# Kernel optimization log

Hardware: AMD Instinct MI355X
Metric: run time of the kernel (lower is better)

## Reference

```python
import jax, jax.numpy as jnp
import numpy as np

N_NODES = 100000
N_EDGES = 1600000
IN_CH = 128


def _sage_conv(x, src, dst, Wl, b, Wr, n_nodes):
    # PyG SAGEConv (aggr='mean', root_weight=True):
    #   out_i = lin_l(mean_{j->i} x_j) + lin_r(x_i)
    msg = x[src]                                             # [E, F]
    agg = jax.ops.segment_sum(msg, dst, num_segments=n_nodes)  # [N, F]
    deg = jax.ops.segment_sum(jnp.ones((src.shape[0],), x.dtype), dst,
                              num_segments=n_nodes)          # [N]
    mean = agg / jnp.maximum(deg, 1.0)[:, None]
    return mean @ Wl + b + x @ Wr


def setup_inputs() -> dict:
    key = jax.random.key(0)
    ks = jax.random.split(key, 10)
    x = jax.random.normal(ks[0], (N_NODES, IN_CH), dtype=jnp.float32)
    edge_index = jax.random.randint(ks[1], (2, N_EDGES), 0, N_NODES, dtype=jnp.int64)
    s = 0.05
    return {
        "x": x,
        "edge_index": edge_index,
        "W1l": jax.random.normal(ks[2], (IN_CH, 32), dtype=jnp.float32) * s,
        "b1": jax.random.normal(ks[3], (32,), dtype=jnp.float32) * s,
        "W1r": jax.random.normal(ks[4], (IN_CH, 32), dtype=jnp.float32) * s,
        "W2l": jax.random.normal(ks[5], (32, 16), dtype=jnp.float32) * s,
        "b2": jax.random.normal(ks[6], (16,), dtype=jnp.float32) * s,
        "W2r": jax.random.normal(ks[7], (32, 16), dtype=jnp.float32) * s,
        "Wfc": jax.random.normal(ks[8], (16, 2), dtype=jnp.float32) * s,
        "bfc": jax.random.normal(ks[9], (2,), dtype=jnp.float32) * s,
    }


def reference(x, edge_index, W1l, b1, W1r, W2l, b2, W2r, Wfc, bfc):
    src, dst = edge_index[0], edge_index[1]
    n = x.shape[0]
    h = jax.nn.relu(_sage_conv(x, src, dst, W1l, b1, W1r, n))   # [N, 32]
    h = jax.nn.relu(_sage_conv(h, src, dst, W2l, b2, W2r, n))   # [N, 16]
    return h @ Wfc + bfc                                        # [N, 2]
```

## Files before the change

### kernel.cpp

```cpp
#include <hip/hip_runtime.h>

#define TPB 256
#define BK_SHIFT 7
#define BK_SIZE 128
#define NBK_MAX 800
#define EPT 32
#define CAP 3072

typedef __attribute__((ext_vector_type(8))) short bf16x8;
typedef __attribute__((ext_vector_type(4))) float f32x4;

__device__ __forceinline__ unsigned short f2bf(float f) {
    unsigned u = __float_as_uint(f);
    unsigned r = (u + 0x7FFFu + ((u >> 16) & 1u)) >> 16;
    return (unsigned short)r;
}
__device__ __forceinline__ float bf2f(unsigned short b) {
    return __uint_as_float((unsigned)b << 16);
}
__device__ __forceinline__ void acc4(float4& a, ushort4 v) {
    a.x += bf2f(v.x); a.y += bf2f(v.y); a.z += bf2f(v.z); a.w += bf2f(v.w);
}

__global__ __launch_bounds__(256) void hist_buckets(
    const int* __restrict__ dst, int* __restrict__ bcnt, int E, int NBK)
{
    __shared__ int h[NBK_MAX];
    const int t = threadIdx.x;
    for (int i = t; i < NBK; i += 256) h[i] = 0;
    __syncthreads();
    const int E4 = E >> 2;
    for (int e4 = blockIdx.x * blockDim.x + t; e4 < E4; e4 += gridDim.x * blockDim.x) {
        int4 d = ((const int4*)dst)[e4];
        atomicAdd(&h[d.x >> BK_SHIFT], 1);
        atomicAdd(&h[d.y >> BK_SHIFT], 1);
        atomicAdd(&h[d.z >> BK_SHIFT], 1);
        atomicAdd(&h[d.w >> BK_SHIFT], 1);
    }
    if (blockIdx.x == 0) {
        for (int e = E4 * 4 + t; e < E; e += 256)
            atomicAdd(&h[dst[e] >> BK_SHIFT], 1);
    }
    __syncthreads();
    for (int i = t; i < NBK; i += 256)
        if (h[i]) atomicAdd(&bcnt[i], h[i]);
}

__global__ __launch_bounds__(1024) void scan_buckets(
    const int* __restrict__ bcnt, int* __restrict__ bbase,
    int* __restrict__ gcursor, int NBK)
{
    __shared__ int s[1024];
    const int t = threadIdx.x;
    int v = (t < NBK) ? bcnt[t] : 0;
    s[t] = v;
    __syncthreads();
    for (int off = 1; off < 1024; off <<= 1) {
        int u = (t >= off) ? s[t - off] : 0;
        __syncthreads();
        s[t] += u;
        __syncthreads();
    }
    if (t < NBK) {
        int excl = s[t] - v;
        bbase[t]   = excl;
        gcursor[t] = excl;
    }
}

__global__ __launch_bounds__(256) void bin_scatter(
    const int* __restrict__ src, const int* __restrict__ dst,
    int* __restrict__ gcursor, int* __restrict__ pk, int E, int NBK)
{
    __shared__ int lcnt[NBK_MAX];
    __shared__ int lbase[NBK_MAX];
    __shared__ int lrank[NBK_MAX];
    const int t = threadIdx.x;
    const int e0 = blockIdx.x * (256 * EPT);

    for (int i = t; i < NBK; i += 256) { lcnt[i] = 0; lrank[i] = 0; }
    __syncthreads();

    #pragma unroll 4
    for (int k = 0; k < EPT; ++k) {
        int e = e0 + k * 256 + t;
        if (e < E) atomicAdd(&lcnt[dst[e] >> BK_SHIFT], 1);
    }
    __syncthreads();

    for (int i = t; i < NBK; i += 256) {
        int c = lcnt[i];
        if (c) lbase[i] = atomicAdd(&gcursor[i], c);
    }
    __syncthreads();

    #pragma unroll 4
    for (int k = 0; k < EPT; ++k) {
        int e = e0 + k * 256 + t;
        if (e < E) {
            int d = dst[e], s = src[e];
            int b = d >> BK_SHIFT;
            int r = atomicAdd(&lrank[b], 1);
            pk[lbase[b] + r] = (s << BK_SHIFT) | (d & (BK_SIZE - 1));
        }
    }
}

__global__ __launch_bounds__(256) void gemm1_mfma(
    const float* __restrict__ A,
    const float* __restrict__ Wl,
    const float* __restrict__ Wr,
    const float* __restrict__ b,
    unsigned short* __restrict__ Yb,
    float* __restrict__ C,
    int N)
{
    const int lane = threadIdx.x & 63;
    const int m    = lane & 15;
    const int quad = lane >> 4;
    const int wave   = blockIdx.x * (blockDim.x >> 6) + (threadIdx.x >> 6);
    const int nwaves = gridDim.x * (blockDim.x >> 6);
    const int ntiles = (N + 15) >> 4;

    bf16x8 Bf[4][4];
    #pragma unroll
    for (int kc = 0; kc < 4; ++kc) {
        #pragma unroll
        for (int jt = 0; jt < 4; ++jt) {
            const float* W = (jt < 2) ? Wl : Wr;
            const int col = (jt & 1) * 16 + m;
            #pragma unroll
            for (int j = 0; j < 8; ++j) {
                int k = kc * 32 + quad * 8 + j;
                Bf[kc][jt][j] = (short)f2bf(W[k * 32 + col]);
            }
        }
    }

    const float bias0 = b[m];
    const float bias1 = b[16 + m];

    for (int tile = wave; tile < ntiles; tile += nwaves) {
        const int node0 = tile * 16;
        const int gn = node0 + m;
        const bool okA = gn < N;
        const float* rowp = A + (size_t)gn * 128;

        bf16x8 Af[4];
        #pragma unroll
        for (int kc = 0; kc < 4; ++kc) {
            float4 v0 = make_float4(0.f, 0.f, 0.f, 0.f);
            float4 v1 = make_float4(0.f, 0.f, 0.f, 0.f);
            if (okA) {
                v0 = *(const float4*)&rowp[kc * 32 + quad * 8];
                v1 = *(const float4*)&rowp[kc * 32 + quad * 8 + 4];
            }
            Af[kc][0] = (short)f2bf(v0.x); Af[kc][1] = (short)f2bf(v0.y);
            Af[kc][2] = (short)f2bf(v0.z); Af[kc][3] = (short)f2bf(v0.w);
            Af[kc][4] = (short)f2bf(v1.x); Af[kc][5] = (short)f2bf(v1.y);
            Af[kc][6] = (short)f2bf(v1.z); Af[kc][7] = (short)f2bf(v1.w);
        }

        f32x4 acc[4] = {{0.f,0.f,0.f,0.f},{0.f,0.f,0.f,0.f},
                        {0.f,0.f,0.f,0.f},{0.f,0.f,0.f,0.f}};
        #pragma unroll
        for (int kc = 0; kc < 4; ++kc) {
            #pragma unroll
            for (int jt = 0; jt < 4; ++jt)
                acc[jt] = __builtin_amdgcn_mfma_f32_16x16x32_bf16(
                    Af[kc], Bf[kc][jt], acc[jt], 0, 0, 0);
        }

        const int nodeBase = node0 + quad * 4;
        #pragma unroll
        for (int reg = 0; reg < 4; ++reg) {
            const int node = nodeBase + reg;
            if (node < N) {
                Yb[(size_t)node * 32 + m]      = f2bf(acc[0][reg]);
                Yb[(size_t)node * 32 + 16 + m] = f2bf(acc[1][reg]);
                C [(size_t)node * 32 + m]      = acc[2][reg] + bias0;
                C [(size_t)node * 32 + 16 + m] = acc[3][reg] + bias1;
            }
        }
    }
}

__global__ __launch_bounds__(256) void gather_gemm2(
    const int* __restrict__ bbase, const int* __restrict__ bcnt,
    const int* __restrict__ pk,
    const unsigned short* __restrict__ Yb,
    const float* __restrict__ c1,
    const float* __restrict__ W2l, const float* __restrict__ W2r,
    const float* __restrict__ b2,
    float* __restrict__ invdeg,
    unsigned short* __restrict__ y2b, float* __restrict__ c2, int N)
{
    __shared__ int lcnt[BK_SIZE];
    __shared__ int soff[BK_SIZE];
    __shared__ int wcur[BK_SIZE];
    __shared__ int sidx[CAP];

    const int t = threadIdx.x;
    const int b = blockIdx.x;
    const int base = bbase[b];
    const int cnt  = min(bcnt[b], CAP);
    const int node0 = b * BK_SIZE;

    if (t < BK_SIZE) lcnt[t] = 0;
    __syncthreads();

    for (int j = t; j < cnt; j += 256)
        atomicAdd(&lcnt[pk[base + j] & (BK_SIZE - 1)], 1);
    __syncthreads();

    int v = (t < BK_SIZE) ? lcnt[t] : 0;
    if (t < BK_SIZE) soff[t] = v;
    __syncthreads();
    for (int off = 1; off < BK_SIZE; off <<= 1) {
        int u = (t < BK_SIZE && t >= off) ? soff[t - off] : 0;
        __syncthreads();
        if (t < BK_SIZE) soff[t] += u;
        __syncthreads();
    }
    if (t < BK_SIZE) wcur[t] = soff[t] - v;
    __syncthreads();

    for (int j = t; j < cnt; j += 256) {
        int pv = pk[base + j];
        int d  = pv & (BK_SIZE - 1);
        int pos = atomicAdd(&wcur[d], 1);
        sidx[pos] = pv >> BK_SHIFT;
    }
    __syncthreads();

    const int q = t & 7;
    #pragma unroll
    for (int pass = 0; pass < 4; ++pass) {
        const int nl = pass * 32 + (t >> 3);
        const int node = node0 + nl;
        const bool active = node < N;
        float h[4] = {0.f, 0.f, 0.f, 0.f};
        if (active) {
            const int deg = lcnt[nl];
            const int en  = soff[nl];
            const int st  = en - deg;
            const float w = 1.0f / fmaxf((float)deg, 1.0f);
            if (q == 0) invdeg[node] = w;

            float4 a0 = make_float4(0.f,0.f,0.f,0.f);
            float4 a1 = make_float4(0.f,0.f,0.f,0.f);
            float4 a2 = make_float4(0.f,0.f,0.f,0.f);
            float4 a3 = make_float4(0.f,0.f,0.f,0.f);
            int j = st;
            for (; j + 3 < en; j += 4) {
                int s0 = sidx[j], s1 = sidx[j+1], s2 = sidx[j+2], s3 = sidx[j+3];
                ushort4 v0 = *(const ushort4*)&Yb[(size_t)s0 * 32 + q * 4];
                ushort4 v1 = *(const ushort4*)&Yb[(size_t)s1 * 32 + q * 4];
                ushort4 v2 = *(const ushort4*)&Yb[(size_t)s2 * 32 + q * 4];
                ushort4 v3 = *(const ushort4*)&Yb[(size_t)s3 * 32 + q * 4];
                acc4(a0, v0); acc4(a1, v1); acc4(a2, v2); acc4(a3, v3);
            }
            for (; j < en; ++j) {
                ushort4 vv = *(const ushort4*)&Yb[(size_t)sidx[j] * 32 + q * 4];
                acc4(a0, vv);
            }
            float4 acc;
            acc.x = (a0.x + a1.x) + (a2.x + a3.x);
            acc.y = (a0.y + a1.y) + (a2.y + a3.y);
            acc.z = (a0.z + a1.z) + (a2.z + a3.z);
            acc.w = (a0.w + a1.w) + (a2.w + a3.w);

            float4 c = *(const float4*)&c1[(size_t)node * 32 + q * 4];
            h[0] = fmaxf(c.x + acc.x * w, 0.f);
            h[1] = fmaxf(c.y + acc.y * w, 0.f);
            h[2] = fmaxf(c.z + acc.z * w, 0.f);
            h[3] = fmaxf(c.w + acc.w * w, 0.f);
        }

        const int  j0  = q * 4;
        const bool isY = (j0 < 16);
        const int  jj  = isY ? j0 : (j0 - 16);
        const float* Wb = isY ? W2l : W2r;

        float o0 = 0.f, o1 = 0.f, o2 = 0.f, o3 = 0.f;
        #pragma unroll
        for (int k = 0; k < 32; ++k) {
            float hk = __shfl(h[k & 3], k >> 2, 8);
            float4 wv = *(const float4*)&Wb[k * 16 + jj];
            o0 += hk * wv.x; o1 += hk * wv.y; o2 += hk * wv.z; o3 += hk * wv.w;
        }

        if (active) {
            if (isY) {
                ushort4 r;
                r.x = f2bf(o0); r.y = f2bf(o1); r.z = f2bf(o2); r.w = f2bf(o3);
                *(ushort4*)&y2b[(size_t)node * 16 + jj] = r;
            } else {
                float4 bb = *(const float4*)&b2[jj];
                *(float4*)&c2[(size_t)node * 16 + jj] =
                    make_float4(o0 + bb.x, o1 + bb.y, o2 + bb.z, o3 + bb.w);
            }
        }
    }
}

__global__ __launch_bounds__(256) void gather_final(
    const int* __restrict__ bbase, const int* __restrict__ bcnt,
    const int* __restrict__ pk,
    const unsigned short* __restrict__ Yb,
    const float* __restrict__ c2,
    const float* __restrict__ invdeg,
    const float* __restrict__ Wfc,
    const float* __restrict__ bfc,
    float* __restrict__ out, int N)
{
    __shared__ int lcnt[BK_SIZE];
    __shared__ int soff[BK_SIZE];
    __shared__ int wcur[BK_SIZE];
    __shared__ int sidx[CAP];

    const int t = threadIdx.x;
    const int b = blockIdx.x;
    const int base = bbase[b];
    const int cnt  = min(bcnt[b], CAP);
    const int node0 = b * BK_SIZE;

    if (t < BK_SIZE) lcnt[t] = 0;
    __syncthreads();

    for (int j = t; j < cnt; j += 256)
        atomicAdd(&lcnt[pk[base + j] & (BK_SIZE - 1)], 1);
    __syncthreads();

    int v = (t < BK_SIZE) ? lcnt[t] : 0;
    if (t < BK_SIZE) soff[t] = v;
    __syncthreads();
    for (int off = 1; off < BK_SIZE; off <<= 1) {
        int u = (t < BK_SIZE && t >= off) ? soff[t - off] : 0;
        __syncthreads();
        if (t < BK_SIZE) soff[t] += u;
        __syncthreads();
    }
    if (t < BK_SIZE) wcur[t] = soff[t] - v;
    __syncthreads();

    for (int j = t; j < cnt; j += 256) {
        int pv = pk[base + j];
        int d  = pv & (BK_SIZE - 1);
        int pos = atomicAdd(&wcur[d], 1);
        sidx[pos] = pv >> BK_SHIFT;
    }
    __syncthreads();

    const int q = t & 3;
    #pragma unroll
    for (int pass = 0; pass < 2; ++pass) {
        const int nl = pass * 64 + (t >> 2);
        const int node = node0 + nl;
        if (node < N) {
            const int deg = lcnt[nl];
            const int en  = soff[nl];
            const int st  = en - deg;
            const float w = invdeg[node];

            float4 a0 = make_float4(0.f,0.f,0.f,0.f);
            float4 a1 = make_float4(0.f,0.f,0.f,0.f);
            float4 a2 = make_float4(0.f,0.f,0.f,0.f);
            float4 a3 = make_float4(0.f,0.f,0.f,0.f);
            int j = st;
            for (; j + 3 < en; j += 4) {
                int s0 = sidx[j], s1 = sidx[j+1], s2 = sidx[j+2], s3 = sidx[j+3];
                ushort4 v0 = *(const ushort4*)&Yb[(size_t)s0 * 16 + q * 4];
                ushort4 v1 = *(const ushort4*)&Yb[(size_t)s1 * 16 + q * 4];
                ushort4 v2 = *(const ushort4*)&Yb[(size_t)s2 * 16 + q * 4];
                ushort4 v3 = *(const ushort4*)&Yb[(size_t)s3 * 16 + q * 4];
                acc4(a0, v0); acc4(a1, v1); acc4(a2, v2); acc4(a3, v3);
            }
            for (; j < en; ++j) {
                ushort4 vv = *(const ushort4*)&Yb[(size_t)sidx[j] * 16 + q * 4];
                acc4(a0, vv);
            }
            float4 acc;
            acc.x = (a0.x + a1.x) + (a2.x + a3.x);
            acc.y = (a0.y + a1.y) + (a2.y + a3.y);
            acc.z = (a0.z + a1.z) + (a2.z + a3.z);
            acc.w = (a0.w + a1.w) + (a2.w + a3.w);

            float4 c = *(const float4*)&c2[(size_t)node * 16 + q * 4];
            float h0 = fmaxf(c.x + acc.x * w, 0.f);
            float h1 = fmaxf(c.y + acc.y * w, 0.f);
            float h2 = fmaxf(c.z + acc.z * w, 0.f);
            float h3 = fmaxf(c.w + acc.w * w, 0.f);

            const float* Wq = &Wfc[q * 8];
            float o0 = h0 * Wq[0] + h1 * Wq[2] + h2 * Wq[4] + h3 * Wq[6];
            float o1 = h0 * Wq[1] + h1 * Wq[3] + h2 * Wq[5] + h3 * Wq[7];

            o0 += __shfl_xor(o0, 1); o0 += __shfl_xor(o0, 2);
            o1 += __shfl_xor(o1, 1); o1 += __shfl_xor(o1, 2);

            if (q == 0) ((float2*)out)[node] = make_float2(o0 + bfc[0], o1 + bfc[1]);
        } else {
            float z = 0.f;
            z += __shfl_xor(z, 1); z += __shfl_xor(z, 2);
        }
    }
}

extern "C" void kernel_launch(void* const* d_in, const int* in_sizes, int n_in,
                              void* d_out, int out_size, void* d_ws, size_t ws_size,
                              hipStream_t stream)
{
    const float* x   = (const float*)d_in[0];
    const int*   ei  = (const int*)d_in[1];
    const float* W1l = (const float*)d_in[2];
    const float* b1  = (const float*)d_in[3];
    const float* W1r = (const float*)d_in[4];
    const float* W2l = (const float*)d_in[5];
    const float* b2  = (const float*)d_in[6];
    const float* W2r = (const float*)d_in[7];
    const float* Wfc = (const float*)d_in[8];
    const float* bfc = (const float*)d_in[9];
    float* out = (float*)d_out;

    const int N = in_sizes[0] / 128;
    const int E = in_sizes[1] / 2;
    const int* src = ei;
    const int* dst = ei + E;

    const int NBK = (N + BK_SIZE - 1) / BK_SIZE;

    int*   bucket_cnt  = (int*)d_ws;
    int*   bucket_base = bucket_cnt + NBK_MAX;
    int*   gcursor     = bucket_base + NBK_MAX;
    float* invdeg      = (float*)(gcursor + NBK_MAX);
    int*   pk          = (int*)(invdeg + N);
    unsigned short* y1b = (unsigned short*)(pk + E);
    float* c1          = (float*)(y1b + (size_t)N * 32);
    unsigned short* y2b = (unsigned short*)(c1 + (size_t)N * 32);
    float* c2          = (float*)(y2b + (size_t)N * 16);

    hipMemsetAsync(bucket_cnt, 0, (size_t)NBK * sizeof(int), stream);
    hist_buckets<<<196, 256, 0, stream>>>(dst, bucket_cnt, E, NBK);
    scan_buckets<<<1, 1024, 0, stream>>>(bucket_cnt, bucket_base, gcursor, NBK);
    {
        int nb = (E + 256 * EPT - 1) / (256 * EPT);
        bin_scatter<<<nb, 256, 0, stream>>>(src, dst, gcursor, pk, E, NBK);
    }

    gemm1_mfma<<<256, TPB, 0, stream>>>(x, W1l, W1r, b1, y1b, c1, N);

    gather_gemm2<<<NBK, TPB, 0, stream>>>(
        bucket_base, bucket_cnt, pk, y1b, c1, W2l, W2r, b2,
        invdeg, y2b, c2, N);

    gather_final<<<NBK, TPB, 0, stream>>>(
        bucket_base, bucket_cnt, pk, y2b, c2, invdeg, Wfc, bfc, out, N);
}
```

Measured before the change: 214.1 us.

## Replace bucketed edge binning with per-node global CSR built via atomics

Swaps the 128-node bucket binning, which both gather kernels re-sorted in shared memory, for a full per-node CSR. A global per-node histogram, a block-level scan with an atomic global base, and an atomic scatter produce it once. The gather kernels then read row_start/degree directly, drop their per-block shared-memory sort and the invdeg buffer, and launch many more small blocks. The cost is about 3.2M global atomics on 100K counters, with contention and scattered writes, and node rows are no longer placed in ascending node order.

```diff
diff --git a/kernel.cpp b/kernel.cpp
--- a/kernel.cpp
+++ b/kernel.cpp
@@ -1,11 +1,6 @@
 #include <hip/hip_runtime.h>
 
 #define TPB 256
-#define BK_SHIFT 7
-#define BK_SIZE 128
-#define NBK_MAX 800
-#define EPT 32
-#define CAP 3072
 
 typedef __attribute__((ext_vector_type(8))) short bf16x8;
 typedef __attribute__((ext_vector_type(4))) float f32x4;
@@ -22,86 +17,69 @@
     a.x += bf2f(v.x); a.y += bf2f(v.y); a.z += bf2f(v.z); a.w += bf2f(v.w);
 }
 
-__global__ __launch_bounds__(256) void hist_buckets(
-    const int* __restrict__ dst, int* __restrict__ bcnt, int E, int NBK)
-{
-    __shared__ int h[NBK_MAX];
+__global__ __launch_bounds__(256) void hist_nodes(
+    const int* __restrict__ dst, int* __restrict__ ncnt, int E)
+{
+    const int E4 = E >> 2;
+    for (int e4 = blockIdx.x * blockDim.x + threadIdx.x; e4 < E4;
+         e4 += gridDim.x * blockDim.x) {
+        int4 d = ((const int4*)dst)[e4];
+        atomicAdd(&ncnt[d.x], 1);
+        atomicAdd(&ncnt[d.y], 1);
+        atomicAdd(&ncnt[d.z], 1);
+        atomicAdd(&ncnt[d.w], 1);
+    }
+    if (blockIdx.x == 0) {
+        for (int e = E4 * 4 + threadIdx.x; e < E; e += 256)
+            atomicAdd(&ncnt[dst[e]], 1);
+    }
+}
+
+__global__ __launch_bounds__(256) void node_offsets(
+    const int* __restrict__ ncnt, int* __restrict__ gcur,
+    int* __restrict__ row_start, int* __restrict__ ncursor, int N)
+{
+    __shared__ int s[256];
+    __shared__ int base;
     const int t = threadIdx.x;
-    for (int i = t; i < NBK; i += 256) h[i] = 0;
+    const int node = blockIdx.x * 256 + t;
+    int c = (node < N) ? ncnt[node] : 0;
+    s[t] = c;
     __syncthreads();
-    const int E4 = E >> 2;
-    for (int e4 = blockIdx.x * blockDim.x + t; e4 < E4; e4 += gridDim.x * blockDim.x) {
-        int4 d = ((const int4*)dst)[e4];
-        atomicAdd(&h[d.x >> BK_SHIFT], 1);
-        atomicAdd(&h[d.y >> BK_SHIFT], 1);
-        atomicAdd(&h[d.z >> BK_SHIFT], 1);
-        atomicAdd(&h[d.w >> BK_SHIFT], 1);
-    }
-    if (blockIdx.x == 0) {
-        for (int e = E4 * 4 + t; e < E; e += 256)
-            atomicAdd(&h[dst[e] >> BK_SHIFT], 1);
-    }
-    __syncthreads();
-    for (int i = t; i < NBK; i += 256)
-        if (h[i]) atomicAdd(&bcnt[i], h[i]);
-}
-
-__global__ __launch_bounds__(1024) void scan_buckets(
-    const int* __restrict__ bcnt, int* __restrict__ bbase,
-    int* __restrict__ gcursor, int NBK)
-{
-    __shared__ int s[1024];
-    const int t = threadIdx.x;
-    int v = (t < NBK) ? bcnt[t] : 0;
-    s[t] = v;
-    __syncthreads();
-    for (int off = 1; off < 1024; off <<= 1) {
+    #pragma unroll
+    for (int off = 1; off < 256; off <<= 1) {
         int u = (t >= off) ? s[t - off] : 0;
         __syncthreads();
         s[t] += u;
         __syncthreads();
     }
-    if (t < NBK) {
-        int excl = s[t] - v;
-        bbase[t]   = excl;
-        gcursor[t] = excl;
-    }
-}
-
-__global__ __launch_bounds__(256) void bin_scatter(
+    if (t == 255) base = atomicAdd(gcur, s[255]);
+    __syncthreads();
+    if (node < N) {
+        int rs = base + s[t] - c;
+        row_start[node] = rs;
+        ncursor[node]   = rs;
+    }
+}
+
+__global__ __launch_bounds__(256) void scatter_csr(
     const int* __restrict__ src, const int* __restrict__ dst,
-    int* __restrict__ gcursor, int* __restrict__ pk, int E, int NBK)
-{
-    __shared__ int lcnt[NBK_MAX];
-    __shared__ int lbase[NBK_MAX];
-    __shared__ int lrank[NBK_MAX];
-    const int t = threadIdx.x;
-    const int e0 = blockIdx.x * (256 * EPT);
-
-    for (int i = t; i < NBK; i += 256) { lcnt[i] = 0; lrank[i] = 0; }
-    __syncthreads();
-
-    #pragma unroll 4
-    for (int k = 0; k < EPT; ++k) {
-        int e = e0 + k * 256 + t;
-        if (e < E) atomicAdd(&lcnt[dst[e] >> BK_SHIFT], 1);
-    }
-    __syncthreads();
-
-    for (int i = t; i < NBK; i += 256) {
-        int c = lcnt[i];
-        if (c) lbase[i] = atomicAdd(&gcursor[i], c);
-    }
-    __syncthreads();
-
-    #pragma unroll 4
-    for (int k = 0; k < EPT; ++k) {
-        int e = e0 + k * 256 + t;
-        if (e < E) {
-            int d = dst[e], s = src[e];
-            int b = d >> BK_SHIFT;
-            int r = atomicAdd(&lrank[b], 1);
-            pk[lbase[b] + r] = (s << BK_SHIFT) | (d & (BK_SIZE - 1));
+    int* __restrict__ ncursor, int* __restrict__ esrc, int E)
+{
+    const int E4 = E >> 2;
+    for (int e4 = blockIdx.x * blockDim.x + threadIdx.x; e4 < E4;
+         e4 += gridDim.x * blockDim.x) {
+        int4 s = ((const int4*)src)[e4];
+        int4 d = ((const int4*)dst)[e4];
+        esrc[atomicAdd(&ncursor[d.x], 1)] = s.x;
+        esrc[atomicAdd(&ncursor[d.y], 1)] = s.y;
+        esrc[atomicAdd(&ncursor[d.z], 1)] = s.z;
+        esrc[atomicAdd(&ncursor[d.w], 1)] = s.w;
+    }
+    if (blockIdx.x == 0) {
+        for (int e = E4 * 4 + threadIdx.x; e < E; e += 256) {
+            int d = dst[e];
+            esrc[atomicAdd(&ncursor[d], 1)] = src[e];
         }
     }
 }
@@ -186,224 +164,140 @@
 }
 
 __global__ __launch_bounds__(256) void gather_gemm2(
-    const int* __restrict__ bbase, const int* __restrict__ bcnt,
-    const int* __restrict__ pk,
+    const int* __restrict__ row_start, const int* __restrict__ ncnt,
+    const int* __restrict__ esrc,
     const unsigned short* __restrict__ Yb,
     const float* __restrict__ c1,
     const float* __restrict__ W2l, const float* __restrict__ W2r,
     const float* __restrict__ b2,
-    float* __restrict__ invdeg,
     unsigned short* __restrict__ y2b, float* __restrict__ c2, int N)
 {
-    __shared__ int lcnt[BK_SIZE];
-    __shared__ int soff[BK_SIZE];
-    __shared__ int wcur[BK_SIZE];
-    __shared__ int sidx[CAP];
-
     const int t = threadIdx.x;
-    const int b = blockIdx.x;
-    const int base = bbase[b];
-    const int cnt  = min(bcnt[b], CAP);
-    const int node0 = b * BK_SIZE;
-
-    if (t < BK_SIZE) lcnt[t] = 0;
-    __syncthreads();
-
-    for (int j = t; j < cnt; j += 256)
-        atomicAdd(&lcnt[pk[base + j] & (BK_SIZE - 1)], 1);
-    __syncthreads();
-
-    int v = (t < BK_SIZE) ? lcnt[t] : 0;
-    if (t < BK_SIZE) soff[t] = v;
-    __syncthreads();
-    for (int off = 1; off < BK_SIZE; off <<= 1) {
-        int u = (t < BK_SIZE && t >= off) ? soff[t - off] : 0;
-        __syncthreads();
-        if (t < BK_SIZE) soff[t] += u;
-        __syncthreads();
-    }
-    if (t < BK_SIZE) wcur[t] = soff[t] - v;
-    __syncthreads();
-
-    for (int j = t; j < cnt; j += 256) {
-        int pv = pk[base + j];
-        int d  = pv & (BK_SIZE - 1);
-        int pos = atomicAdd(&wcur[d], 1);
-        sidx[pos] = pv >> BK_SHIFT;
-    }
-    __syncthreads();
-
     const int q = t & 7;
+    const int node = blockIdx.x * 32 + (t >> 3);
+    const bool active = node < N;
+
+    float h[4] = {0.f, 0.f, 0.f, 0.f};
+    if (active) {
+        const int st  = row_start[node];
+        const int deg = ncnt[node];
+        const int en  = st + deg;
+        const float w = 1.0f / fmaxf((float)deg, 1.0f);
+
+        float4 a0 = make_float4(0.f,0.f,0.f,0.f);
+        float4 a1 = make_float4(0.f,0.f,0.f,0.f);
+        float4 a2 = make_float4(0.f,0.f,0.f,0.f);
+        float4 a3 = make_float4(0.f,0.f,0.f,0.f);
+        int j = st;
+        for (; j + 3 < en; j += 4) {
+            int s0 = esrc[j], s1 = esrc[j+1], s2 = esrc[j+2], s3 = esrc[j+3];
+            ushort4 v0 = *(const ushort4*)&Yb[(size_t)s0 * 32 + q * 4];
+            ushort4 v1 = *(const ushort4*)&Yb[(size_t)s1 * 32 + q * 4];
+            ushort4 v2 = *(const ushort4*)&Yb[(size_t)s2 * 32 + q * 4];
+            ushort4 v3 = *(const ushort4*)&Yb[(size_t)s3 * 32 + q * 4];
+            acc4(a0, v0); acc4(a1, v1); acc4(a2, v2); acc4(a3, v3);
+        }
+        for (; j < en; ++j) {
+            ushort4 vv = *(const ushort4*)&Yb[(size_t)esrc[j] * 32 + q * 4];
+            acc4(a0, vv);
+        }
+        float4 acc;
+        acc.x = (a0.x + a1.x) + (a2.x + a3.x);
+        acc.y = (a0.y + a1.y) + (a2.y + a3.y);
+        acc.z = (a0.z + a1.z) + (a2.z + a3.z);
+        acc.w = (a0.w + a1.w) + (a2.w + a3.w);
+
+        float4 c = *(const float4*)&c1[(size_t)node * 32 + q * 4];
+        h[0] = fmaxf(c.x + acc.x * w, 0.f);
+        h[1] = fmaxf(c.y + acc.y * w, 0.f);
+        h[2] = fmaxf(c.z + acc.z * w, 0.f);
+        h[3] = fmaxf(c.w + acc.w * w, 0.f);
+    }
+
+    const int  j0  = q * 4;
+    const bool isY = (j0 < 16);
+    const int  jj  = isY ? j0 : (j0 - 16);
+    const float* Wb = isY ? W2l : W2r;
+
+    float o0 = 0.f, o1 = 0.f, o2 = 0.f, o3 = 0.f;
     #pragma unroll
-    for (int pass = 0; pass < 4; ++pass) {
-        const int nl = pass * 32 + (t >> 3);
-        const int node = node0 + nl;
-        const bool active = node < N;
-        float h[4] = {0.f, 0.f, 0.f, 0.f};
-        if (active) {
-            const int deg = lcnt[nl];
-            const int en  = soff[nl];
-            const int st  = en - deg;
-            const float w = 1.0f / fmaxf((float)deg, 1.0f);
-            if (q == 0) invdeg[node] = w;
-
-            float4 a0 = make_float4(0.f,0.f,0.f,0.f);
-            float4 a1 = make_float4(0.f,0.f,0.f,0.f);
-            float4 a2 = make_float4(0.f,0.f,0.f,0.f);
-            float4 a3 = make_float4(0.f,0.f,0.f,0.f);
-            int j = st;
-            for (; j + 3 < en; j += 4) {
-                int s0 = sidx[j], s1 = sidx[j+1], s2 = sidx[j+2], s3 = sidx[j+3];
-                ushort4 v0 = *(const ushort4*)&Yb[(size_t)s0 * 32 + q * 4];
-                ushort4 v1 = *(const ushort4*)&Yb[(size_t)s1 * 32 + q * 4];
-                ushort4 v2 = *(const ushort4*)&Yb[(size_t)s2 * 32 + q * 4];
-                ushort4 v3 = *(const ushort4*)&Yb[(size_t)s3 * 32 + q * 4];
-                acc4(a0, v0); acc4(a1, v1); acc4(a2, v2); acc4(a3, v3);
-            }
-            for (; j < en; ++j) {
-                ushort4 vv = *(const ushort4*)&Yb[(size_t)sidx[j] * 32 + q * 4];
-                acc4(a0, vv);
-            }
-            float4 acc;
-            acc.x = (a0.x + a1.x) + (a2.x + a3.x);
-            acc.y = (a0.y + a1.y) + (a2.y + a3.y);
-            acc.z = (a0.z + a1.z) + (a2.z + a3.z);
-            acc.w = (a0.w + a1.w) + (a2.w + a3.w);
-
-            float4 c = *(const float4*)&c1[(size_t)node * 32 + q * 4];
-            h[0] = fmaxf(c.x + acc.x * w, 0.f);
-            h[1] = fmaxf(c.y + acc.y * w, 0.f);
-            h[2] = fmaxf(c.z + acc.z * w, 0.f);
-            h[3] = fmaxf(c.w + acc.w * w, 0.f);
-        }
-
-        const int  j0  = q * 4;
-        const bool isY = (j0 < 16);
-        const int  jj  = isY ? j0 : (j0 - 16);
-        const float* Wb = isY ? W2l : W2r;
-
-        float o0 = 0.f, o1 = 0.f, o2 = 0.f, o3 = 0.f;
-        #pragma unroll
-        for (int k = 0; k < 32; ++k) {
-            float hk = __shfl(h[k & 3], k >> 2, 8);
-            float4 wv = *(const float4*)&Wb[k * 16 + jj];
-            o0 += hk * wv.x; o1 += hk * wv.y; o2 += hk * wv.z; o3 += hk * wv.w;
-        }
-
-        if (active) {
-            if (isY) {
-                ushort4 r;
-                r.x = f2bf(o0); r.y = f2bf(o1); r.z = f2bf(o2); r.w = f2bf(o3);
-                *(ushort4*)&y2b[(size_t)node * 16 + jj] = r;
-            } else {
-                float4 bb = *(const float4*)&b2[jj];
-                *(float4*)&c2[(size_t)node * 16 + jj] =
-                    make_float4(o0 + bb.x, o1 + bb.y, o2 + bb.z, o3 + bb.w);
-            }
+    for (int k = 0; k < 32; ++k) {
+        float hk = __shfl(h[k & 3], k >> 2, 8);
+        float4 wv = *(const float4*)&Wb[k * 16 + jj];
+        o0 += hk * wv.x; o1 += hk * wv.y; o2 += hk * wv.z; o3 += hk * wv.w;
+    }
+
+    if (active) {
+        if (isY) {
+            ushort4 r;
+            r.x = f2bf(o0); r.y = f2bf(o1); r.z = f2bf(o2); r.w = f2bf(o3);
+            *(ushort4*)&y2b[(size_t)node * 16 + jj] = r;
+        } else {
+            float4 bb = *(const float4*)&b2[jj];
+            *(float4*)&c2[(size_t)node * 16 + jj] =
+                make_float4(o0 + bb.x, o1 + bb.y, o2 + bb.z, o3 + bb.w);
         }
     }
 }
 
 __global__ __launch_bounds__(256) void gather_final(
-    const int* __restrict__ bbase, const int* __restrict__ bcnt,
-    const int* __restrict__ pk,
+    const int* __restrict__ row_start, const int* __restrict__ ncnt,
+    const int* __restrict__ esrc,
     const unsigned short* __restrict__ Yb,
     const float* __restrict__ c2,
-    const float* __restrict__ invdeg,
     const float* __restrict__ Wfc,
     const float* __restrict__ bfc,
     float* __restrict__ out, int N)
 {
-    __shared__ int lcnt[BK_SIZE];
-    __shared__ int soff[BK_SIZE];
-    __shared__ int wcur[BK_SIZE];
-    __shared__ int sidx[CAP];
-
     const int t = threadIdx.x;
-    const int b = blockIdx.x;
-    const int base = bbase[b];
-    const int cnt  = min(bcnt[b], CAP);
-    const int node0 = b * BK_SIZE;
-
-    if (t < BK_SIZE) lcnt[t] = 0;
-    __syncthreads();
-
-    for (int j = t; j < cnt; j += 256)
-        atomicAdd(&lcnt[pk[base + j] & (BK_SIZE - 1)], 1);
-    __syncthreads();
-
-    int v = (t < BK_SIZE) ? lcnt[t] : 0;
-    if (t < BK_SIZE) soff[t] = v;
-    __syncthreads();
-    for (int off = 1; off < BK_SIZE; off <<= 1) {
-        int u = (t < BK_SIZE && t >= off) ? soff[t - off] : 0;
-        __syncthreads();
-        if (t < BK_SIZE) soff[t] += u;
-        __syncthreads();
-    }
-    if (t < BK_SIZE) wcur[t] = soff[t] - v;
-    __syncthreads();
-
-    for (int j = t; j < cnt; j += 256) {
-        int pv = pk[base + j];
-        int d  = pv & (BK_SIZE - 1);
-        int pos = atomicAdd(&wcur[d], 1);
-        sidx[pos] = pv >> BK_SHIFT;
-    }
-    __syncthreads();
-
     const int q = t & 3;
-    #pragma unroll
-    for (int pass = 0; pass < 2; ++pass) {
-        const int nl = pass * 64 + (t >> 2);
-        const int node = node0 + nl;
-        if (node < N) {
-            const int deg = lcnt[nl];
-            const int en  = soff[nl];
-            const int st  = en - deg;
-            const float w = invdeg[node];
-
-            float4 a0 = make_float4(0.f,0.f,0.f,0.f);
-            float4 a1 = make_float4(0.f,0.f,0.f,0.f);
-            float4 a2 = make_float4(0.f,0.f,0.f,0.f);
-            float4 a3 = make_float4(0.f,0.f,0.f,0.f);
-            int j = st;
-            for (; j + 3 < en; j += 4) {
-                int s0 = sidx[j], s1 = sidx[j+1], s2 = sidx[j+2], s3 = sidx[j+3];
-                ushort4 v0 = *(const ushort4*)&Yb[(size_t)s0 * 16 + q * 4];
-                ushort4 v1 = *(const ushort4*)&Yb[(size_t)s1 * 16 + q * 4];
-                ushort4 v2 = *(const ushort4*)&Yb[(size_t)s2 * 16 + q * 4];
-                ushort4 v3 = *(const ushort4*)&Yb[(size_t)s3 * 16 + q * 4];
-                acc4(a0, v0); acc4(a1, v1); acc4(a2, v2); acc4(a3, v3);
-            }
-            for (; j < en; ++j) {
-                ushort4 vv = *(const ushort4*)&Yb[(size_t)sidx[j] * 16 + q * 4];
-                acc4(a0, vv);
-            }
-            float4 acc;
-            acc.x = (a0.x + a1.x) + (a2.x + a3.x);
-            acc.y = (a0.y + a1.y) + (a2.y + a3.y);
-            acc.z = (a0.z + a1.z) + (a2.z + a3.z);
-            acc.w = (a0.w + a1.w) + (a2.w + a3.w);
-
-            float4 c = *(const float4*)&c2[(size_t)node * 16 + q * 4];
-            float h0 = fmaxf(c.x + acc.x * w, 0.f);
-            float h1 = fmaxf(c.y + acc.y * w, 0.f);
-            float h2 = fmaxf(c.z + acc.z * w, 0.f);
-            float h3 = fmaxf(c.w + acc.w * w, 0.f);
-
-            const float* Wq = &Wfc[q * 8];
-            float o0 = h0 * Wq[0] + h1 * Wq[2] + h2 * Wq[4] + h3 * Wq[6];
-            float o1 = h0 * Wq[1] + h1 * Wq[3] + h2 * Wq[5] + h3 * Wq[7];
-
-            o0 += __shfl_xor(o0, 1); o0 += __shfl_xor(o0, 2);
-            o1 += __shfl_xor(o1, 1); o1 += __shfl_xor(o1, 2);
-
-            if (q == 0) ((float2*)out)[node] = make_float2(o0 + bfc[0], o1 + bfc[1]);
-        } else {
-            float z = 0.f;
-            z += __shfl_xor(z, 1); z += __shfl_xor(z, 2);
-        }
+    const int node = blockIdx.x * 64 + (t >> 2);
+    if (node < N) {
+        const int st  = row_start[node];
+        const int deg = ncnt[node];
+        const int en  = st + deg;
+        const float w = 1.0f / fmaxf((float)deg, 1.0f);
+
+        float4 a0 = make_float4(0.f,0.f,0.f,0.f);
+        float4 a1 = make_float4(0.f,0.f,0.f,0.f);
+        float4 a2 = make_float4(0.f,0.f,0.f,0.f);
+        float4 a3 = make_float4(0.f,0.f,0.f,0.f);
+        int j = st;
+        for (; j + 3 < en; j += 4) {
+            int s0 = esrc[j], s1 = esrc[j+1], s2 = esrc[j+2], s3 = esrc[j+3];
+            ushort4 v0 = *(const ushort4*)&Yb[(size_t)s0 * 16 + q * 4];
+            ushort4 v1 = *(const ushort4*)&Yb[(size_t)s1 * 16 + q * 4];
+            ushort4 v2 = *(const ushort4*)&Yb[(size_t)s2 * 16 + q * 4];
+            ushort4 v3 = *(const ushort4*)&Yb[(size_t)s3 * 16 + q * 4];
+            acc4(a0, v0); acc4(a1, v1); acc4(a2, v2); acc4(a3, v3);
+        }
+        for (; j < en; ++j) {
+            ushort4 vv = *(const ushort4*)&Yb[(size_t)esrc[j] * 16 + q * 4];
+            acc4(a0, vv);
+        }
+        float4 acc;
+        acc.x = (a0.x + a1.x) + (a2.x + a3.x);
+        acc.y = (a0.y + a1.y) + (a2.y + a3.y);
+        acc.z = (a0.z + a1.z) + (a2.z + a3.z);
+        acc.w = (a0.w + a1.w) + (a2.w + a3.w);
+
+        float4 c = *(const float4*)&c2[(size_t)node * 16 + q * 4];
+        float h0 = fmaxf(c.x + acc.x * w, 0.f);
+        float h1 = fmaxf(c.y + acc.y * w, 0.f);
+        float h2 = fmaxf(c.z + acc.z * w, 0.f);
+        float h3 = fmaxf(c.w + acc.w * w, 0.f);
+
+        const float* Wq = &Wfc[q * 8];
+        float o0 = h0 * Wq[0] + h1 * Wq[2] + h2 * Wq[4] + h3 * Wq[6];
+        float o1 = h0 * Wq[1] + h1 * Wq[3] + h2 * Wq[5] + h3 * Wq[7];
+
+        o0 += __shfl_xor(o0, 1); o0 += __shfl_xor(o0, 2);
+        o1 += __shfl_xor(o1, 1); o1 += __shfl_xor(o1, 2);
+
+        if (q == 0) ((float2*)out)[node] = make_float2(o0 + bfc[0], o1 + bfc[1]);
+    } else {
+        float z = 0.f;
+        z += __shfl_xor(z, 1); z += __shfl_xor(z, 2);
     }
 }
 
@@ -428,32 +322,26 @@
     const int* src = ei;
     const int* dst = ei + E;
 
-    const int NBK = (N + BK_SIZE - 1) / BK_SIZE;
-
-    int*   bucket_cnt  = (int*)d_ws;
-    int*   bucket_base = bucket_cnt + NBK_MAX;
-    int*   gcursor     = bucket_base + NBK_MAX;
-    float* invdeg      = (float*)(gcursor + NBK_MAX);
-    int*   pk          = (int*)(invdeg + N);
-    unsigned short* y1b = (unsigned short*)(pk + E);
+    int* ncnt      = (int*)d_ws;
+    int* gcur      = ncnt + N;
+    int* row_start = gcur + 8;
+    int* ncursor   = row_start + N;
+    int* esrc      = ncursor + N;
+    unsigned short* y1b = (unsigned short*)(esrc + E);
     float* c1          = (float*)(y1b + (size_t)N * 32);
     unsigned short* y2b = (unsigned short*)(c1 + (size_t)N * 32);
     float* c2          = (float*)(y2b + (size_t)N * 16);
 
-    hipMemsetAsync(bucket_cnt, 0, (size_t)NBK * sizeof(int), stream);
-    hist_buckets<<<196, 256, 0, stream>>>(dst, bucket_cnt, E, NBK);
-    scan_buckets<<<1, 1024, 0, stream>>>(bucket_cnt, bucket_base, gcursor, NBK);
-    {
-        int nb = (E + 256 * EPT - 1) / (256 * EPT);
-        bin_scatter<<<nb, 256, 0, stream>>>(src, dst, gcursor, pk, E, NBK);
-    }
+    hipMemsetAsync(ncnt, 0, ((size_t)N + 8) * sizeof(int), stream);
+    hist_nodes<<<512, 256, 0, stream>>>(dst, ncnt, E);
+    node_offsets<<<(N + 255) / 256, 256, 0, stream>>>(ncnt, gcur, row_start, ncursor, N);
+    scatter_csr<<<512, 256, 0, stream>>>(src, dst, ncursor, esrc, E);
 
     gemm1_mfma<<<256, TPB, 0, stream>>>(x, W1l, W1r, b1, y1b, c1, N);
 
-    gather_gemm2<<<NBK, TPB, 0, stream>>>(
-        bucket_base, bucket_cnt, pk, y1b, c1, W2l, W2r, b2,
-        invdeg, y2b, c2, N);
-
-    gather_final<<<NBK, TPB, 0, stream>>>(
-        bucket_base, bucket_cnt, pk, y2b, c2, invdeg, Wfc, bfc, out, N);
-}
+    gather_gemm2<<<(N + 31) / 32, TPB, 0, stream>>>(
+        row_start, ncnt, esrc, y1b, c1, W2l, W2r, b2, y2b, c2, N);
+
+    gather_final<<<(N + 63) / 64, TPB, 0, stream>>>(
+        row_start, ncnt, esrc, y2b, c2, Wfc, bfc, out, N);
+}
```

After: 345.9 us. 1.62x slower.

## Build CSR once in a bucket-sort kernel and gather from global CSR

Applied to the files above, without the earlier changes.

Adds a bucket_sort kernel that sorts each destination bucket's packed edges in shared memory once and writes a CSR layout (source ids in place, plus row_start and degree per node). Both gather kernels then drop their duplicated per-block local sort and read neighbour lists straight from global memory, with finer-grained grids of 32 or 64 nodes per block. This removes repeating the sort in two kernels and raises parallelism in the gathers. In exchange it adds a kernel launch and an extra read and write pass over the edge array, and the gathers now read indices from global memory instead of LDS.

```diff
diff --git a/kernel.cpp b/kernel.cpp
--- a/kernel.cpp
+++ b/kernel.cpp
@@ -102,6 +102,58 @@
             int b = d >> BK_SHIFT;
             int r = atomicAdd(&lrank[b], 1);
             pk[lbase[b] + r] = (s << BK_SHIFT) | (d & (BK_SIZE - 1));
+        }
+    }
+}
+
+__global__ __launch_bounds__(256) void bucket_sort(
+    const int* __restrict__ bbase, const int* __restrict__ bcnt,
+    int* __restrict__ pk,
+    int* __restrict__ row_start, int* __restrict__ deg, int N)
+{
+    __shared__ int lcnt[BK_SIZE];
+    __shared__ int soff[BK_SIZE];
+    __shared__ int wcur[BK_SIZE];
+    __shared__ int sidx[CAP];
+
+    const int t = threadIdx.x;
+    const int b = blockIdx.x;
+    const int base = bbase[b];
+    const int cnt  = min(bcnt[b], CAP);
+    const int node0 = b * BK_SIZE;
+
+    if (t < BK_SIZE) lcnt[t] = 0;
+    __syncthreads();
+
+    for (int j = t; j < cnt; j += 256)
+        atomicAdd(&lcnt[pk[base + j] & (BK_SIZE - 1)], 1);
+    __syncthreads();
+
+    int v = (t < BK_SIZE) ? lcnt[t] : 0;
+    if (t < BK_SIZE) soff[t] = v;
+    __syncthreads();
+    for (int off = 1; off < BK_SIZE; off <<= 1) {
+        int u = (t < BK_SIZE && t >= off) ? soff[t - off] : 0;
+        __syncthreads();
+        if (t < BK_SIZE) soff[t] += u;
+        __syncthreads();
+    }
+    if (t < BK_SIZE) wcur[t] = soff[t] - v;
+    __syncthreads();
+
+    for (int j = t; j < cnt; j += 256) {
+        int pv = pk[base + j];
+        int pos = atomicAdd(&wcur[pv & (BK_SIZE - 1)], 1);
+        sidx[pos] = pv >> BK_SHIFT;
+    }
+    __syncthreads();
+
+    for (int j = t; j < cnt; j += 256) pk[base + j] = sidx[j];
+    if (t < BK_SIZE) {
+        int node = node0 + t;
+        if (node < N) {
+            row_start[node] = base + soff[t] - v;
+            deg[node]       = v;
         }
     }
 }
@@ -186,224 +238,140 @@
 }
 
 __global__ __launch_bounds__(256) void gather_gemm2(
-    const int* __restrict__ bbase, const int* __restrict__ bcnt,
-    const int* __restrict__ pk,
+    const int* __restrict__ row_start, const int* __restrict__ deg_arr,
+    const int* __restrict__ esrc,
     const unsigned short* __restrict__ Yb,
     const float* __restrict__ c1,
     const float* __restrict__ W2l, const float* __restrict__ W2r,
     const float* __restrict__ b2,
-    float* __restrict__ invdeg,
     unsigned short* __restrict__ y2b, float* __restrict__ c2, int N)
 {
-    __shared__ int lcnt[BK_SIZE];
-    __shared__ int soff[BK_SIZE];
-    __shared__ int wcur[BK_SIZE];
-    __shared__ int sidx[CAP];
-
-    const int t = threadIdx.x;
-    const int b = blockIdx.x;
-    const int base = bbase[b];
-    const int cnt  = min(bcnt[b], CAP);
-    const int node0 = b * BK_SIZE;
-
-    if (t < BK_SIZE) lcnt[t] = 0;
-    __syncthreads();
-
-    for (int j = t; j < cnt; j += 256)
-        atomicAdd(&lcnt[pk[base + j] & (BK_SIZE - 1)], 1);
-    __syncthreads();
-
-    int v = (t < BK_SIZE) ? lcnt[t] : 0;
-    if (t < BK_SIZE) soff[t] = v;
-    __syncthreads();
-    for (int off = 1; off < BK_SIZE; off <<= 1) {
-        int u = (t < BK_SIZE && t >= off) ? soff[t - off] : 0;
-        __syncthreads();
-        if (t < BK_SIZE) soff[t] += u;
-        __syncthreads();
-    }
-    if (t < BK_SIZE) wcur[t] = soff[t] - v;
-    __syncthreads();
-
-    for (int j = t; j < cnt; j += 256) {
-        int pv = pk[base + j];
-        int d  = pv & (BK_SIZE - 1);
-        int pos = atomicAdd(&wcur[d], 1);
-        sidx[pos] = pv >> BK_SHIFT;
-    }
-    __syncthreads();
-
+    const int t = threadIdx.x;
     const int q = t & 7;
+    const int node = blockIdx.x * 32 + (t >> 3);
+    const bool active = node < N;
+
+    float h[4] = {0.f, 0.f, 0.f, 0.f};
+    if (active) {
+        const int st  = row_start[node];
+        const int deg = deg_arr[node];
+        const int en  = st + deg;
+        const float w = 1.0f / fmaxf((float)deg, 1.0f);
+
+        float4 a0 = make_float4(0.f,0.f,0.f,0.f);
+        float4 a1 = make_float4(0.f,0.f,0.f,0.f);
+        float4 a2 = make_float4(0.f,0.f,0.f,0.f);
+        float4 a3 = make_float4(0.f,0.f,0.f,0.f);
+        int j = st;
+        for (; j + 3 < en; j += 4) {
+            int s0 = esrc[j], s1 = esrc[j+1], s2 = esrc[j+2], s3 = esrc[j+3];
+            ushort4 v0 = *(const ushort4*)&Yb[(size_t)s0 * 32 + q * 4];
+            ushort4 v1 = *(const ushort4*)&Yb[(size_t)s1 * 32 + q * 4];
+            ushort4 v2 = *(const ushort4*)&Yb[(size_t)s2 * 32 + q * 4];
+            ushort4 v3 = *(const ushort4*)&Yb[(size_t)s3 * 32 + q * 4];
+            acc4(a0, v0); acc4(a1, v1); acc4(a2, v2); acc4(a3, v3);
+        }
+        for (; j < en; ++j) {
+            ushort4 vv = *(const ushort4*)&Yb[(size_t)esrc[j] * 32 + q * 4];
+            acc4(a0, vv);
+        }
+        float4 acc;
+        acc.x = (a0.x + a1.x) + (a2.x + a3.x);
+        acc.y = (a0.y + a1.y) + (a2.y + a3.y);
+        acc.z = (a0.z + a1.z) + (a2.z + a3.z);
+        acc.w = (a0.w + a1.w) + (a2.w + a3.w);
+
+        float4 c = *(const float4*)&c1[(size_t)node * 32 + q * 4];
+        h[0] = fmaxf(c.x + acc.x * w, 0.f);
+        h[1] = fmaxf(c.y + acc.y * w, 0.f);
+        h[2] = fmaxf(c.z + acc.z * w, 0.f);
+        h[3] = fmaxf(c.w + acc.w * w, 0.f);
+    }
+
+    const int  j0  = q * 4;
+    const bool isY = (j0 < 16);
+    const int  jj  = isY ? j0 : (j0 - 16);
+    const float* Wb = isY ? W2l : W2r;
+
+    float o0 = 0.f, o1 = 0.f, o2 = 0.f, o3 = 0.f;
     #pragma unroll
-    for (int pass = 0; pass < 4; ++pass) {
-        const int nl = pass * 32 + (t >> 3);
-        const int node = node0 + nl;
-        const bool active = node < N;
-        float h[4] = {0.f, 0.f, 0.f, 0.f};
-        if (active) {
-            const int deg = lcnt[nl];
-            const int en  = soff[nl];
-            const int st  = en - deg;
-            const float w = 1.0f / fmaxf((float)deg, 1.0f);
-            if (q == 0) invdeg[node] = w;
-
-            float4 a0 = make_float4(0.f,0.f,0.f,0.f);
-            float4 a1 = make_float4(0.f,0.f,0.f,0.f);
-            float4 a2 = make_float4(0.f,0.f,0.f,0.f);
-            float4 a3 = make_float4(0.f,0.f,0.f,0.f);
-            int j = st;
-            for (; j + 3 < en; j += 4) {
-                int s0 = sidx[j], s1 = sidx[j+1], s2 = sidx[j+2], s3 = sidx[j+3];
-                ushort4 v0 = *(const ushort4*)&Yb[(size_t)s0 * 32 + q * 4];
-                ushort4 v1 = *(const ushort4*)&Yb[(size_t)s1 * 32 + q * 4];
-                ushort4 v2 = *(const ushort4*)&Yb[(size_t)s2 * 32 + q * 4];
-                ushort4 v3 = *(const ushort4*)&Yb[(size_t)s3 * 32 + q * 4];
-                acc4(a0, v0); acc4(a1, v1); acc4(a2, v2); acc4(a3, v3);
-            }
-            for (; j < en; ++j) {
-                ushort4 vv = *(const ushort4*)&Yb[(size_t)sidx[j] * 32 + q * 4];
-                acc4(a0, vv);
-            }
-            float4 acc;
-            acc.x = (a0.x + a1.x) + (a2.x + a3.x);
-            acc.y = (a0.y + a1.y) + (a2.y + a3.y);
-            acc.z = (a0.z + a1.z) + (a2.z + a3.z);
-            acc.w = (a0.w + a1.w) + (a2.w + a3.w);
-
-            float4 c = *(const float4*)&c1[(size_t)node * 32 + q * 4];
-            h[0] = fmaxf(c.x + acc.x * w, 0.f);
-            h[1] = fmaxf(c.y + acc.y * w, 0.f);
-            h[2] = fmaxf(c.z + acc.z * w, 0.f);
-            h[3] = fmaxf(c.w + acc.w * w, 0.f);
-        }
-
-        const int  j0  = q * 4;
-        const bool isY = (j0 < 16);
-        const int  jj  = isY ? j0 : (j0 - 16);
-        const float* Wb = isY ? W2l : W2r;
-
-        float o0 = 0.f, o1 = 0.f, o2 = 0.f, o3 = 0.f;
-        #pragma unroll
-        for (int k = 0; k < 32; ++k) {
-            float hk = __shfl(h[k & 3], k >> 2, 8);
-            float4 wv = *(const float4*)&Wb[k * 16 + jj];
-            o0 += hk * wv.x; o1 += hk * wv.y; o2 += hk * wv.z; o3 += hk * wv.w;
-        }
-
-        if (active) {
-            if (isY) {
-                ushort4 r;
-                r.x = f2bf(o0); r.y = f2bf(o1); r.z = f2bf(o2); r.w = f2bf(o3);
-                *(ushort4*)&y2b[(size_t)node * 16 + jj] = r;
-            } else {
-                float4 bb = *(const float4*)&b2[jj];
-                *(float4*)&c2[(size_t)node * 16 + jj] =
-                    make_float4(o0 + bb.x, o1 + bb.y, o2 + bb.z, o3 + bb.w);
-            }
+    for (int k = 0; k < 32; ++k) {
+        float hk = __shfl(h[k & 3], k >> 2, 8);
+        float4 wv = *(const float4*)&Wb[k * 16 + jj];
+        o0 += hk * wv.x; o1 += hk * wv.y; o2 += hk * wv.z; o3 += hk * wv.w;
+    }
+
+    if (active) {
+        if (isY) {
+            ushort4 r;
+            r.x = f2bf(o0); r.y = f2bf(o1); r.z = f2bf(o2); r.w = f2bf(o3);
+            *(ushort4*)&y2b[(size_t)node * 16 + jj] = r;
+        } else {
+            float4 bb = *(const float4*)&b2[jj];
+            *(float4*)&c2[(size_t)node * 16 + jj] =
+                make_float4(o0 + bb.x, o1 + bb.y, o2 + bb.z, o3 + bb.w);
         }
     }
 }
 
 __global__ __launch_bounds__(256) void gather_final(
-    const int* __restrict__ bbase, const int* __restrict__ bcnt,
-    const int* __restrict__ pk,
+    const int* __restrict__ row_start, const int* __restrict__ deg_arr,
+    const int* __restrict__ esrc,
     const unsigned short* __restrict__ Yb,
     const float* __restrict__ c2,
-    const float* __restrict__ invdeg,
     const float* __restrict__ Wfc,
     const float* __restrict__ bfc,
     float* __restrict__ out, int N)
 {
-    __shared__ int lcnt[BK_SIZE];
-    __shared__ int soff[BK_SIZE];
-    __shared__ int wcur[BK_SIZE];
-    __shared__ int sidx[CAP];
-
-    const int t = threadIdx.x;
-    const int b = blockIdx.x;
-    const int base = bbase[b];
-    const int cnt  = min(bcnt[b], CAP);
-    const int node0 = b * BK_SIZE;
-
-    if (t < BK_SIZE) lcnt[t] = 0;
-    __syncthreads();
-
-    for (int j = t; j < cnt; j += 256)
-        atomicAdd(&lcnt[pk[base + j] & (BK_SIZE - 1)], 1);
-    __syncthreads();
-
-    int v = (t < BK_SIZE) ? lcnt[t] : 0;
-    if (t < BK_SIZE) soff[t] = v;
-    __syncthreads();
-    for (int off = 1; off < BK_SIZE; off <<= 1) {
-        int u = (t < BK_SIZE && t >= off) ? soff[t - off] : 0;
-        __syncthreads();
-        if (t < BK_SIZE) soff[t] += u;
-        __syncthreads();
-    }
-    if (t < BK_SIZE) wcur[t] = soff[t] - v;
-    __syncthreads();
-
-    for (int j = t; j < cnt; j += 256) {
-        int pv = pk[base + j];
-        int d  = pv & (BK_SIZE - 1);
-        int pos = atomicAdd(&wcur[d], 1);
-        sidx[pos] = pv >> BK_SHIFT;
-    }
-    __syncthreads();
-
+    const int t = threadIdx.x;
     const int q = t & 3;
-    #pragma unroll
-    for (int pass = 0; pass < 2; ++pass) {
-        const int nl = pass * 64 + (t >> 2);
-        const int node = node0 + nl;
-        if (node < N) {
-            const int deg = lcnt[nl];
-            const int en  = soff[nl];
-            const int st  = en - deg;
-            const float w = invdeg[node];
-
-            float4 a0 = make_float4(0.f,0.f,0.f,0.f);
-            float4 a1 = make_float4(0.f,0.f,0.f,0.f);
-            float4 a2 = make_float4(0.f,0.f,0.f,0.f);
-            float4 a3 = make_float4(0.f,0.f,0.f,0.f);
-            int j = st;
-            for (; j + 3 < en; j += 4) {
-                int s0 = sidx[j], s1 = sidx[j+1], s2 = sidx[j+2], s3 = sidx[j+3];
-                ushort4 v0 = *(const ushort4*)&Yb[(size_t)s0 * 16 + q * 4];
-                ushort4 v1 = *(const ushort4*)&Yb[(size_t)s1 * 16 + q * 4];
-                ushort4 v2 = *(const ushort4*)&Yb[(size_t)s2 * 16 + q * 4];
-                ushort4 v3 = *(const ushort4*)&Yb[(size_t)s3 * 16 + q * 4];
-                acc4(a0, v0); acc4(a1, v1); acc4(a2, v2); acc4(a3, v3);
-            }
-            for (; j < en; ++j) {
-                ushort4 vv = *(const ushort4*)&Yb[(size_t)sidx[j] * 16 + q * 4];
-                acc4(a0, vv);
-            }
-            float4 acc;
-            acc.x = (a0.x + a1.x) + (a2.x + a3.x);
-            acc.y = (a0.y + a1.y) + (a2.y + a3.y);
-            acc.z = (a0.z + a1.z) + (a2.z + a3.z);
-            acc.w = (a0.w + a1.w) + (a2.w + a3.w);
-
-            float4 c = *(const float4*)&c2[(size_t)node * 16 + q * 4];
-            float h0 = fmaxf(c.x + acc.x * w, 0.f);
-            float h1 = fmaxf(c.y + acc.y * w, 0.f);
-            float h2 = fmaxf(c.z + acc.z * w, 0.f);
-            float h3 = fmaxf(c.w + acc.w * w, 0.f);
-
-            const float* Wq = &Wfc[q * 8];
-            float o0 = h0 * Wq[0] + h1 * Wq[2] + h2 * Wq[4] + h3 * Wq[6];
-            float o1 = h0 * Wq[1] + h1 * Wq[3] + h2 * Wq[5] + h3 * Wq[7];
-
-            o0 += __shfl_xor(o0, 1); o0 += __shfl_xor(o0, 2);
-            o1 += __shfl_xor(o1, 1); o1 += __shfl_xor(o1, 2);
-
-            if (q == 0) ((float2*)out)[node] = make_float2(o0 + bfc[0], o1 + bfc[1]);
-        } else {
-            float z = 0.f;
-            z += __shfl_xor(z, 1); z += __shfl_xor(z, 2);
-        }
+    const int node = blockIdx.x * 64 + (t >> 2);
+    if (node < N) {
+        const int st  = row_start[node];
+        const int deg = deg_arr[node];
+        const int en  = st + deg;
+        const float w = 1.0f / fmaxf((float)deg, 1.0f);
+
+        float4 a0 = make_float4(0.f,0.f,0.f,0.f);
+        float4 a1 = make_float4(0.f,0.f,0.f,0.f);
+        float4 a2 = make_float4(0.f,0.f,0.f,0.f);
+        float4 a3 = make_float4(0.f,0.f,0.f,0.f);
+        int j = st;
+        for (; j + 3 < en; j += 4) {
+            int s0 = esrc[j], s1 = esrc[j+1], s2 = esrc[j+2], s3 = esrc[j+3];
+            ushort4 v0 = *(const ushort4*)&Yb[(size_t)s0 * 16 + q * 4];
+            ushort4 v1 = *(const ushort4*)&Yb[(size_t)s1 * 16 + q * 4];
+            ushort4 v2 = *(const ushort4*)&Yb[(size_t)s2 * 16 + q * 4];
+            ushort4 v3 = *(const ushort4*)&Yb[(size_t)s3 * 16 + q * 4];
+            acc4(a0, v0); acc4(a1, v1); acc4(a2, v2); acc4(a3, v3);
+        }
+        for (; j < en; ++j) {
+            ushort4 vv = *(const ushort4*)&Yb[(size_t)esrc[j] * 16 + q * 4];
+            acc4(a0, vv);
+        }
+        float4 acc;
+        acc.x = (a0.x + a1.x) + (a2.x + a3.x);
+        acc.y = (a0.y + a1.y) + (a2.y + a3.y);
+        acc.z = (a0.z + a1.z) + (a2.z + a3.z);
+        acc.w = (a0.w + a1.w) + (a2.w + a3.w);
+
+        float4 c = *(const float4*)&c2[(size_t)node * 16 + q * 4];
+        float h0 = fmaxf(c.x + acc.x * w, 0.f);
+        float h1 = fmaxf(c.y + acc.y * w, 0.f);
+        float h2 = fmaxf(c.z + acc.z * w, 0.f);
+        float h3 = fmaxf(c.w + acc.w * w, 0.f);
+
+        const float* Wq = &Wfc[q * 8];
+        float o0 = h0 * Wq[0] + h1 * Wq[2] + h2 * Wq[4] + h3 * Wq[6];
+        float o1 = h0 * Wq[1] + h1 * Wq[3] + h2 * Wq[5] + h3 * Wq[7];
+
+        o0 += __shfl_xor(o0, 1); o0 += __shfl_xor(o0, 2);
+        o1 += __shfl_xor(o1, 1); o1 += __shfl_xor(o1, 2);
+
+        if (q == 0) ((float2*)out)[node] = make_float2(o0 + bfc[0], o1 + bfc[1]);
+    } else {
+        float z = 0.f;
+        z += __shfl_xor(z, 1); z += __shfl_xor(z, 2);
     }
 }
 
@@ -433,8 +401,9 @@
     int*   bucket_cnt  = (int*)d_ws;
     int*   bucket_base = bucket_cnt + NBK_MAX;
     int*   gcursor     = bucket_base + NBK_MAX;
-    float* invdeg      = (float*)(gcursor + NBK_MAX);
-    int*   pk          = (int*)(invdeg + N);
+    int*   row_start   = gcursor + NBK_MAX;
+    int*   deg         = row_start + N;
+    int*   pk          = deg + N;
     unsigned short* y1b = (unsigned short*)(pk + E);
     float* c1          = (float*)(y1b + (size_t)N * 32);
     unsigned short* y2b = (unsigned short*)(c1 + (size_t)N * 32);
@@ -447,13 +416,14 @@
         int nb = (E + 256 * EPT - 1) / (256 * EPT);
         bin_scatter<<<nb, 256, 0, stream>>>(src, dst, gcursor, pk, E, NBK);
     }
+    bucket_sort<<<NBK, 256, 0, stream>>>(bucket_base, bucket_cnt, pk,
+                                         row_start, deg, N);
 
     gemm1_mfma<<<256, TPB, 0, stream>>>(x, W1l, W1r, b1, y1b, c1, N);
 
-    gather_gemm2<<<NBK, TPB, 0, stream>>>(
-        bucket_base, bucket_cnt, pk, y1b, c1, W2l, W2r, b2,
-        invdeg, y2b, c2, N);
-
-    gather_final<<<NBK, TPB, 0, stream>>>(
-        bucket_base, bucket_cnt, pk, y2b, c2, invdeg, Wfc, bfc, out, N);
-}
+    gather_gemm2<<<(N + 31) / 32, TPB, 0, stream>>>(
+        row_start, deg, pk, y1b, c1, W2l, W2r, b2, y2b, c2, N);
+
+    gather_final<<<(N + 63) / 64, TPB, 0, stream>>>(
+        row_start, deg, pk, y2b, c2, Wfc, bfc, out, N);
+}
```

After: 220.5 us. +3.0%, slower.
